# Kernel tuning notes

Hardware: AMD Instinct MI355X
Metric: run time of the kernel (lower is better)

The kernel has to match this reference:

```python
import jax, jax.numpy as jnp
import numpy as np

B, S, HID, NH = 2, 2048, 1024, 16
HD = HID // NH
BASE = 10000.0


def _rope_tables(seq_len, head_dim):
    i = jnp.arange(0, head_dim, 2, dtype=jnp.float32)
    theta = BASE ** (-i / head_dim)
    pos = jnp.arange(seq_len, dtype=jnp.float32)
    m_theta = jnp.outer(pos, theta)  # [S, HD/2]
    cos = jnp.repeat(jnp.cos(m_theta), 2, axis=1)  # [S, HD]
    sin = jnp.repeat(jnp.sin(m_theta), 2, axis=1)
    return cos, sin


def _apply_rope(x, cos, sin):
    # x: [B, NH, S, HD]; interleaved rotation: (-x1, x0, -x3, x2, ...)
    x_even = x[..., 0::2]
    x_odd = x[..., 1::2]
    inv_x = jnp.stack((-x_odd, x_even), axis=-1).reshape(x.shape)
    return x * cos[None, None] + inv_x * sin[None, None]


def setup_inputs() -> dict:
    key = jax.random.key(0)
    ks = jax.random.split(key, 7)
    q = jax.random.normal(ks[0], (B, S, HID), dtype=jnp.float32)
    k = jax.random.normal(ks[1], (B, S, HID), dtype=jnp.float32)
    v = jax.random.normal(ks[2], (B, S, HID), dtype=jnp.float32)
    scale = 1.0 / np.sqrt(HID)
    Wq = jax.random.normal(ks[3], (HID, HID), dtype=jnp.float32) * scale
    Wk = jax.random.normal(ks[4], (HID, HID), dtype=jnp.float32) * scale
    Wv = jax.random.normal(ks[5], (HID, HID), dtype=jnp.float32) * scale
    Wo = jax.random.normal(ks[6], (HID, HID), dtype=jnp.float32) * scale
    mask = jnp.triu(jnp.ones((S, S), dtype=bool), k=1)[None, None]  # causal, True = masked
    return {"q": q, "k": k, "v": v, "mask": mask,
            "Wq": Wq, "Wk": Wk, "Wv": Wv, "Wo": Wo}


def reference(q, k, v, mask, Wq, Wk, Wv, Wo):
    cos, sin = _rope_tables(S, HD)
    # Linear (torch stores weight as [out, in]; y = x @ W.T)
    qh = (q @ Wq.T).reshape(B, S, NH, HD).transpose(0, 2, 1, 3)
    kh = (k @ Wk.T).reshape(B, S, NH, HD).transpose(0, 2, 1, 3)
    vh = (v @ Wv.T).reshape(B, S, NH, HD).transpose(0, 2, 1, 3)
    qh = _apply_rope(qh, cos, sin)
    kh = _apply_rope(kh, cos, sin)
    scores = jnp.einsum("bhqd,bhkd->bhqk", qh, kh) / np.sqrt(HD)
    neg_min = jnp.finfo(jnp.float32).min
    scores = jnp.where(mask, neg_min, scores)
    attn = jax.nn.softmax(scores, axis=-1)
    out = jnp.einsum("bhqk,bhkd->bhqd", attn, vh)  # [B,NH,S,HD]
    out = out.transpose(0, 2, 1, 3).reshape(B, S, HID)
    return out @ Wo.T
```

## Files before the change

kernel.cpp:

```cpp
#include <hip/hip_runtime.h>

#define S_LEN 2048
#define HIDN  1024
#define NHEAD 16
#define HDIM  64
#define MROWS 4096
#define KDIM  1024
#define NDIM  1024

typedef __attribute__((ext_vector_type(8))) short bf16x8;
typedef __attribute__((ext_vector_type(4))) short bf16x4;
typedef __attribute__((ext_vector_type(4))) float f32x4;

static __device__ __forceinline__ ushort f2bf(float f) {
    unsigned int u = __float_as_uint(f);
    u = (u + 0x7fffu + ((u >> 16) & 1u)) >> 16;
    return (ushort)u;
}
static __device__ __forceinline__ float bf2f(ushort u) {
    return __uint_as_float(((unsigned int)u) << 16);
}

static __device__ __forceinline__ void gload16(const ushort* g, ushort* l) {
    __builtin_amdgcn_global_load_lds(
        (const __attribute__((address_space(1))) unsigned int*)g,
        (__attribute__((address_space(3))) unsigned int*)l, 16, 0, 0);
}

__global__ __launch_bounds__(256) void prep_kernel(
    const float* __restrict__ q, const float* __restrict__ k,
    const float* __restrict__ v, const float* __restrict__ Wq,
    const float* __restrict__ Wk, const float* __restrict__ Wv,
    const float* __restrict__ Wo,
    ushort* __restrict__ qb, ushort* __restrict__ kb, ushort* __restrict__ vb,
    ushort* __restrict__ Wqb, ushort* __restrict__ Wkb, ushort* __restrict__ Wvb,
    ushort* __restrict__ Wob,
    float* __restrict__ rc, float* __restrict__ rs)
{
    const long Q4 = (long)MROWS * KDIM / 4;
    const long W4 = (long)NDIM * KDIM / 4;
    if (blockIdx.x < 16384) {
        long i = (long)blockIdx.x * 256 + threadIdx.x;
        const float* src; ushort* dst; long off;
        if (i < Q4)          { src = q; dst = qb; off = i; }
        else if (i < 2 * Q4) { src = k; dst = kb; off = i - Q4; }
        else if (i < 3 * Q4) { src = v; dst = vb; off = i - 2 * Q4; }
        else {
            long t = i - 3 * Q4;
            int wsel = (int)(t >> 18);
            off = t & (W4 - 1);
            src = (wsel == 0) ? Wq : (wsel == 1) ? Wk : (wsel == 2) ? Wv : Wo;
            dst = (wsel == 0) ? Wqb : (wsel == 1) ? Wkb : (wsel == 2) ? Wvb : Wob;
        }
        float4 vv = ((const float4*)src)[off];
        ushort4 o;
        o.x = f2bf(vv.x); o.y = f2bf(vv.y); o.z = f2bf(vv.z); o.w = f2bf(vv.w);
        ((ushort4*)dst)[off] = o;
    } else {
        int idx = (blockIdx.x - 16384) * 256 + threadIdx.x;
        int s  = idx >> 5;
        int jp = idx & 31;
        float theta = expf(-(float)(2 * jp) * (9.210340371976184f / 64.0f));
        float ang = (float)s * theta;
        float sv, cv;
        sincosf(ang, &sv, &cv);
        rc[idx] = cv;
        rs[idx] = sv;
    }
}

static __device__ __forceinline__ void gemm_mainloop128(
    const ushort* __restrict__ A, const ushort* __restrict__ W,
    ushort* As, ushort* Bs, f32x4 (&acc)[4][4],
    int m0, int n0, int tid)
{
    const int lane = tid & 63, wid = tid >> 6;
    const int wm = wid & 1, wn = wid >> 1;
    const int quad = lane >> 4, l15 = lane & 15;

    for (int k0 = 0; k0 < KDIM; k0 += 64) {
        __syncthreads();
#pragma unroll
        for (int rr = 0; rr < 4; ++rr) {
            int sidx = tid + rr * 256;
            int row = sidx >> 3;
            int g = (sidx & 7) ^ (row & 7);
            gload16(A + (size_t)(m0 + row) * KDIM + k0 + g * 8, As + sidx * 8);
            gload16(W + (size_t)(n0 + row) * KDIM + k0 + g * 8, Bs + sidx * 8);
        }
        __syncthreads();

#pragma unroll
        for (int ks = 0; ks < 2; ++ks) {
            bf16x8 af[4], bfr[4];
#pragma unroll
            for (int i = 0; i < 4; ++i) {
                int row = wm * 64 + i * 16 + l15;
                int gg = ((ks << 2) | quad) ^ (row & 7);
                af[i] = *(const bf16x8*)&As[row * 64 + gg * 8];
            }
#pragma unroll
            for (int j = 0; j < 4; ++j) {
                int row = wn * 64 + j * 16 + l15;
                int gg = ((ks << 2) | quad) ^ (row & 7);
                bfr[j] = *(const bf16x8*)&Bs[row * 64 + gg * 8];
            }
#pragma unroll
            for (int i = 0; i < 4; ++i)
#pragma unroll
                for (int j = 0; j < 4; ++j)
                    acc[i][j] = __builtin_amdgcn_mfma_f32_16x16x32_bf16(
                        af[i], bfr[j], acc[i][j], 0, 0, 0);
        }
    }
}

__global__ __launch_bounds__(256, 3) void gemm_qkv(
    const ushort* __restrict__ qb, const ushort* __restrict__ kb,
    const ushort* __restrict__ vb,
    const ushort* __restrict__ Wqb, const ushort* __restrict__ Wkb,
    const ushort* __restrict__ Wvb,
    ushort* __restrict__ Qh, ushort* __restrict__ Kh, ushort* __restrict__ Vt,
    const float* __restrict__ rc, const float* __restrict__ rs)
{
    __shared__ __align__(16) ushort As[128 * 64];
    __shared__ __align__(16) ushort Bs[128 * 64];

    const int tid = threadIdx.x;
    const int lane = tid & 63, wid = tid >> 6;
    const int wm = wid & 1, wn = wid >> 1;
    const int quad = lane >> 4, l15 = lane & 15;
    const int z = blockIdx.z;

    const ushort* A; const ushort* W; int m0, n0;
    if (z == 2) {
        m0 = (int)blockIdx.y * 128;
        n0 = (int)blockIdx.x * 128;
        A = Wvb; W = vb;
    } else {
        m0 = blockIdx.x * 128; n0 = blockIdx.y * 128;
        A = (z == 0) ? qb : kb;
        W = (z == 0) ? Wqb : Wkb;
    }

    f32x4 acc[4][4];
#pragma unroll
    for (int i = 0; i < 4; ++i)
#pragma unroll
        for (int j = 0; j < 4; ++j) acc[i][j] = 0.0f;

    gemm_mainloop128(A, W, As, Bs, acc, m0, n0, tid);

    if (z != 2) {
        ushort* out = (z == 0) ? Qh : Kh;
        const float scale = (z == 0) ? 0.18033688011112042f : 1.0f;
#pragma unroll
        for (int i = 0; i < 4; ++i)
#pragma unroll
            for (int j = 0; j < 4; ++j)
#pragma unroll
                for (int r = 0; r < 4; ++r) {
                    int m = m0 + wm * 64 + i * 16 + quad * 4 + r;
                    int n = n0 + wn * 64 + j * 16 + l15;
                    float v = acc[i][j][r];
                    int b = m >> 11, s = m & (S_LEN - 1);
                    int h = n >> 6, d = n & 63;
                    int pidx = s * 32 + (d >> 1);
                    float cv = rc[pidx], sv = rs[pidx];
                    float partner = __shfl_xor(v, 1);
                    v = (d & 1) ? (v * cv + partner * sv)
                                : (v * cv - partner * sv);
                    out[((size_t)((b * NHEAD + h) * S_LEN + s)) * HDIM + d] =
                        f2bf(v * scale);
                }
    } else {
#pragma unroll
        for (int i = 0; i < 4; ++i)
#pragma unroll
            for (int j = 0; j < 4; ++j)
#pragma unroll
                for (int r = 0; r < 4; ++r) {
                    int m = m0 + wm * 64 + i * 16 + quad * 4 + r;
                    int n = n0 + wn * 64 + j * 16 + l15;
                    int h = m >> 6, d = m & 63;
                    int b = n >> 11, s = n & (S_LEN - 1);
                    Vt[((size_t)((b * NHEAD + h) * HDIM + d)) * S_LEN + s] =
                        f2bf(acc[i][j][r]);
                }
    }
}

__global__ __launch_bounds__(256) void gemm_out(
    const ushort* __restrict__ O0, const ushort* __restrict__ O1,
    const float* __restrict__ L0, const float* __restrict__ L1,
    const ushort* __restrict__ W, float* __restrict__ out)
{
    __shared__ __align__(16) ushort As[64 * 64];
    __shared__ __align__(16) ushort Bs[128 * 64];

    const int tid = threadIdx.x;
    const int lane = tid & 63, wid = tid >> 6;
    const int wm = wid & 1, wn = wid >> 1;
    const int quad = lane >> 4, l15 = lane & 15;
    const int m0 = blockIdx.x * 64, n0 = blockIdx.y * 128;

    f32x4 acc[2][4];
#pragma unroll
    for (int i = 0; i < 2; ++i)
#pragma unroll
        for (int j = 0; j < 4; ++j) acc[i][j] = 0.0f;

    for (int k0 = 0; k0 < KDIM; k0 += 64) {
        const int h = k0 >> 6;
        bf16x8 a0[2], a1[2];
        float li[2];
#pragma unroll
        for (int rr = 0; rr < 2; ++rr) {
            int sidx = tid + rr * 256;
            int row = sidx >> 3;
            int g = (sidx & 7) ^ (row & 7);
            int m = m0 + row, bb = m >> 11, s = m & (S_LEN - 1);
            size_t rowO = (size_t)(bb * NHEAD + h) * S_LEN + s;
            a0[rr] = *(const bf16x8*)(O0 + rowO * HDIM + g * 8);
            a1[rr] = *(const bf16x8*)(O1 + rowO * HDIM + g * 8);
            li[rr] = __builtin_amdgcn_rcpf(L0[rowO] + L1[rowO]);
        }
        __syncthreads();
#pragma unroll
        for (int rr = 0; rr < 2; ++rr) {
            int sidx = tid + rr * 256;
            bf16x8 packed;
#pragma unroll
            for (int e = 0; e < 8; ++e) {
                float f = (bf2f((ushort)a0[rr][e]) + bf2f((ushort)a1[rr][e])) * li[rr];
                packed[e] = (short)(__float_as_uint(f) >> 16);
            }
            *(bf16x8*)&As[sidx * 8] = packed;
        }
#pragma unroll
        for (int rr = 0; rr < 4; ++rr) {
            int sidx = tid + rr * 256;
            int row = sidx >> 3;
            int g = (sidx & 7) ^ (row & 7);
            gload16(W + (size_t)(n0 + row) * KDIM + k0 + g * 8, Bs + sidx * 8);
        }
        __syncthreads();

#pragma unroll
        for (int ks = 0; ks < 2; ++ks) {
            bf16x8 af[2], bfr[4];
#pragma unroll
            for (int i = 0; i < 2; ++i) {
                int row = wm * 32 + i * 16 + l15;
                int gg = ((ks << 2) | quad) ^ (row & 7);
                af[i] = *(const bf16x8*)&As[row * 64 + gg * 8];
            }
#pragma unroll
            for (int j = 0; j < 4; ++j) {
                int row = wn * 64 + j * 16 + l15;
                int gg = ((ks << 2) | quad) ^ (row & 7);
                bfr[j] = *(const bf16x8*)&Bs[row * 64 + gg * 8];
            }
#pragma unroll
            for (int i = 0; i < 2; ++i)
#pragma unroll
                for (int j = 0; j < 4; ++j)
                    acc[i][j] = __builtin_amdgcn_mfma_f32_16x16x32_bf16(
                        af[i], bfr[j], acc[i][j], 0, 0, 0);
        }
    }

#pragma unroll
    for (int i = 0; i < 2; ++i)
#pragma unroll
        for (int j = 0; j < 4; ++j)
#pragma unroll
            for (int r = 0; r < 4; ++r) {
                int m = m0 + wm * 32 + i * 16 + quad * 4 + r;
                int n = n0 + wn * 64 + j * 16 + l15;
                out[(size_t)m * NDIM + n] = acc[i][j][r];
            }
}

__global__ __launch_bounds__(256) void attn_mfma(
    const ushort* __restrict__ Qh, const ushort* __restrict__ Kh,
    const ushort* __restrict__ Vt,
    ushort* __restrict__ O0, ushort* __restrict__ O1,
    float* __restrict__ L0, float* __restrict__ L1)
{
    __shared__ __align__(16) ushort Ks[64 * 64];
    __shared__ __align__(16) ushort Vs[64 * 64];

    const int tid = threadIdx.x;
    const int lane = tid & 63, w = tid >> 6;
    const int quad = lane >> 4, l15 = lane & 15;
    const int id = blockIdx.x;
    const int h = id & 15, b = (id >> 4) & 1, t = id >> 5;

    int seg, y;
    if (t < 32) { seg = (t & 1) ? 0 : 1; y = (t & 1) ? 31 - (t >> 1) : (t >> 1); }
    else { int u = t - 32; seg = (u & 1) ? 0 : 1;
           y = (u & 1) ? 15 - (u >> 1) : 16 + (u >> 1); }

    const int qt = seg ? (31 - y) : y;
    const int lo = seg ? ((33 - y) >> 1) : 0;
    const int hi = seg ? (32 - y) : ((y + 2) >> 1);
    const int q0 = qt * 64;
    const size_t hoff = (size_t)(b * NHEAD + h) * S_LEN * HDIM;

    bf16x8 qf[2];
#pragma unroll
    for (int ks = 0; ks < 2; ++ks)
        qf[ks] = *(const bf16x8*)(Qh + hoff +
            (size_t)(q0 + w * 16 + l15) * HDIM + ks * 32 + quad * 8);

    f32x4 Oa[4];
#pragma unroll
    for (int mt = 0; mt < 4; ++mt) Oa[mt] = 0.0f;
    float lsum = 0.f;
    const int myq = q0 + w * 16 + l15;

    const ushort* kg[2];
    const ushort* vgr[2];
    int vwa[2][2];
#pragma unroll
    for (int rr = 0; rr < 2; ++rr) {
        int sidx = tid + rr * 256;
        int row = sidx >> 3;
        int gsw = (sidx & 7) ^ (row & 7);
        kg[rr] = Kh + hoff + (size_t)(lo * 64 + row) * HDIM + gsw * 8;
        int sp = sidx & 7;
        vgr[rr] = Vt + hoff + (size_t)row * S_LEN + lo * 64 + sp * 8;
        vwa[rr][0] = row * 64 + ((2 * sp)     ^ (row & 15)) * 4;
        vwa[rr][1] = row * 64 + ((2 * sp + 1) ^ (row & 15)) * 4;
    }

    bf16x8 vv[2];
    if (lo < hi) {
#pragma unroll
        for (int rr = 0; rr < 2; ++rr) { vv[rr] = *(const bf16x8*)vgr[rr]; vgr[rr] += 64; }
    }

    for (int kt = lo; kt < hi; ++kt) {
        const int k0 = kt * 64;
        const bool diag = (kt == qt);
        __syncthreads();
#pragma unroll
        for (int rr = 0; rr < 2; ++rr) {
            *(bf16x4*)&Vs[vwa[rr][0]] =
                __builtin_shufflevector(vv[rr], vv[rr], 0, 1, 2, 3);
            *(bf16x4*)&Vs[vwa[rr][1]] =
                __builtin_shufflevector(vv[rr], vv[rr], 4, 5, 6, 7);
            gload16(kg[rr], Ks + (tid + rr * 256) * 8);
            kg[rr] += 64 * HDIM;
        }
        if (kt + 1 < hi) {
#pragma unroll
            for (int rr = 0; rr < 2; ++rr) { vv[rr] = *(const bf16x8*)vgr[rr]; vgr[rr] += 64; }
        }
        __syncthreads();

        f32x4 Sa[4];
#pragma unroll
        for (int jm = 0; jm < 4; ++jm) Sa[jm] = 0.0f;
        __builtin_amdgcn_s_setprio(1);
#pragma unroll
        for (int ks = 0; ks < 2; ++ks) {
            const int p = ((ks << 2) | quad) ^ (l15 & 7);
            bf16x8 kf[4];
#pragma unroll
            for (int jm = 0; jm < 4; ++jm)
                kf[jm] = *(const bf16x8*)&Ks[(jm * 16 + l15) * 64 + p * 8];
#pragma unroll
            for (int jm = 0; jm < 4; ++jm)
                Sa[jm] = __builtin_amdgcn_mfma_f32_16x16x32_bf16(
                    kf[jm], qf[ks], Sa[jm], 0, 0, 0);
        }
        __builtin_amdgcn_s_setprio(0);

        bf16x4 pb[4];
#pragma unroll
        for (int jm = 0; jm < 4; ++jm) {
#pragma unroll
            for (int r = 0; r < 4; ++r) {
                float pv = __builtin_amdgcn_exp2f(Sa[jm][r]);
                if (diag) {
                    int key = k0 + jm * 16 + quad * 4 + r;
                    if (key > myq) pv = 0.f;
                }
                lsum += pv;
                pb[jm][r] = (short)(__float_as_uint(pv) >> 16);
            }
        }

        __builtin_amdgcn_s_setprio(1);
#pragma unroll
        for (int jm = 0; jm < 4; ++jm) {
            const int slot = (((jm * 4 + quad) ^ l15) << 2);
#pragma unroll
            for (int mt = 0; mt < 4; ++mt) {
                bf16x4 vf = *(const bf16x4*)&Vs[(mt * 16 + l15) * 64 + slot];
                Oa[mt] = __builtin_amdgcn_mfma_f32_16x16x16bf16_1k(vf, pb[jm],
                                                                   Oa[mt], 0, 0, 0);
            }
        }
        __builtin_amdgcn_s_setprio(0);
    }

    lsum += __shfl_xor(lsum, 16);
    lsum += __shfl_xor(lsum, 32);

    ushort* Op = seg ? O1 : O0;
    float*  Lp = seg ? L1 : L0;
    const size_t row = (size_t)(b * NHEAD + h) * S_LEN + myq;
#pragma unroll
    for (int mt = 0; mt < 4; ++mt) {
        ushort4 o;
        o.x = f2bf(Oa[mt][0]); o.y = f2bf(Oa[mt][1]);
        o.z = f2bf(Oa[mt][2]); o.w = f2bf(Oa[mt][3]);
        *(ushort4*)&Op[row * HDIM + mt * 16 + quad * 4] = o;
    }
    if (quad == 0) Lp[row] = lsum;
}

extern "C" void kernel_launch(void* const* d_in, const int* in_sizes, int n_in,
                              void* d_out, int out_size, void* d_ws, size_t ws_size,
                              hipStream_t stream) {
    const float* qf  = (const float*)d_in[0];
    const float* kf  = (const float*)d_in[1];
    const float* vf  = (const float*)d_in[2];
    const float* Wqf = (const float*)d_in[4];
    const float* Wkf = (const float*)d_in[5];
    const float* Wvf = (const float*)d_in[6];
    const float* Wof = (const float*)d_in[7];
    float* out = (float*)d_out;

    char* wsp = (char*)d_ws;
    float* rc = (float*)wsp;            wsp += 65536 * 4;
    float* rs = (float*)wsp;            wsp += 65536 * 4;
    ushort* qb  = (ushort*)wsp;         wsp += (size_t)MROWS * KDIM * 2;
    ushort* kb  = (ushort*)wsp;         wsp += (size_t)MROWS * KDIM * 2;
    ushort* vb  = (ushort*)wsp;         wsp += (size_t)MROWS * KDIM * 2;
    ushort* Wqb = (ushort*)wsp;         wsp += (size_t)NDIM * KDIM * 2;
    ushort* Wkb = (ushort*)wsp;         wsp += (size_t)NDIM * KDIM * 2;
    ushort* Wvb = (ushort*)wsp;         wsp += (size_t)NDIM * KDIM * 2;
    ushort* Wob = (ushort*)wsp;         wsp += (size_t)NDIM * KDIM * 2;
    ushort* Qh  = (ushort*)wsp;         wsp += (size_t)MROWS * HIDN * 2;
    ushort* Kh  = (ushort*)wsp;         wsp += (size_t)MROWS * HIDN * 2;
    ushort* Vt  = (ushort*)wsp;

    ushort* O0 = qb;
    ushort* O1 = kb;
    float*  L0 = (float*)vb;
    float*  L1 = (float*)vb + 65536;

    prep_kernel<<<16640, 256, 0, stream>>>(qf, kf, vf, Wqf, Wkf, Wvf, Wof,
                                           qb, kb, vb, Wqb, Wkb, Wvb, Wob, rc, rs);

    gemm_qkv<<<dim3(32, 8, 3), 256, 0, stream>>>(
        qb, kb, vb, Wqb, Wkb, Wvb, Qh, Kh, Vt, rc, rs);

    attn_mfma<<<2048, 256, 0, stream>>>(Qh, Kh, Vt, O0, O1, L0, L1);

    gemm_out<<<dim3(64, 8), 256, 0, stream>>>(O0, O1, L0, L1, Wob, out);
}
```

Measured before the change: 207.5 us.

## Split attention tile across waves by query and key halves with LDS reduction

Each of the four waves now handles 32 queries × 32 keys instead of 16 queries × 64 keys. Each K fragment read from LDS is reused by two query tiles and each V fragment by two P tiles, which halves LDS fragment reads per MFMA. The two key-half partial outputs and row sums are combined at the end through an LDS scratch area that reuses the K/V buffers, at the cost of an extra sync and reduction. Launch bounds now also request 4 blocks per CU.

```diff
diff --git a/kernel.cpp b/kernel.cpp
--- a/kernel.cpp
+++ b/kernel.cpp
@@ -282,17 +282,20 @@
             }
 }
 
-__global__ __launch_bounds__(256) void attn_mfma(
+__global__ __launch_bounds__(256, 4) void attn_mfma(
     const ushort* __restrict__ Qh, const ushort* __restrict__ Kh,
     const ushort* __restrict__ Vt,
     ushort* __restrict__ O0, ushort* __restrict__ O1,
     float* __restrict__ L0, float* __restrict__ L1)
 {
-    __shared__ __align__(16) ushort Ks[64 * 64];
-    __shared__ __align__(16) ushort Vs[64 * 64];
+    __shared__ __align__(16) ushort KV[2][64 * 64];
+    __shared__ float lred[4][2][16];
+    ushort* Ks = KV[0];
+    ushort* Vs = KV[1];
 
     const int tid = threadIdx.x;
     const int lane = tid & 63, w = tid >> 6;
+    const int wq = w & 1, wk = w >> 1;
     const int quad = lane >> 4, l15 = lane & 15;
     const int id = blockIdx.x;
     const int h = id & 15, b = (id >> 4) & 1, t = id >> 5;
@@ -308,17 +311,22 @@
     const int q0 = qt * 64;
     const size_t hoff = (size_t)(b * NHEAD + h) * S_LEN * HDIM;
 
-    bf16x8 qf[2];
-#pragma unroll
-    for (int ks = 0; ks < 2; ++ks)
-        qf[ks] = *(const bf16x8*)(Qh + hoff +
-            (size_t)(q0 + w * 16 + l15) * HDIM + ks * 32 + quad * 8);
-
-    f32x4 Oa[4];
-#pragma unroll
-    for (int mt = 0; mt < 4; ++mt) Oa[mt] = 0.0f;
-    float lsum = 0.f;
-    const int myq = q0 + w * 16 + l15;
+    bf16x8 qf[2][2];
+#pragma unroll
+    for (int qn = 0; qn < 2; ++qn)
+#pragma unroll
+        for (int ks = 0; ks < 2; ++ks)
+            qf[qn][ks] = *(const bf16x8*)(Qh + hoff +
+                (size_t)(q0 + wq * 32 + qn * 16 + l15) * HDIM + ks * 32 + quad * 8);
+
+    const int myq0 = q0 + wq * 32 + l15;
+
+    f32x4 Oa[4][2];
+#pragma unroll
+    for (int mt = 0; mt < 4; ++mt)
+#pragma unroll
+        for (int qn = 0; qn < 2; ++qn) Oa[mt][qn] = 0.0f;
+    float lsum[2] = {0.f, 0.f};
 
     const ushort* kg[2];
     const ushort* vgr[2];
@@ -360,67 +368,104 @@
         }
         __syncthreads();
 
-        f32x4 Sa[4];
-#pragma unroll
-        for (int jm = 0; jm < 4; ++jm) Sa[jm] = 0.0f;
+        f32x4 Sa[2][2];
+#pragma unroll
+        for (int jm = 0; jm < 2; ++jm)
+#pragma unroll
+            for (int qn = 0; qn < 2; ++qn) Sa[jm][qn] = 0.0f;
         __builtin_amdgcn_s_setprio(1);
 #pragma unroll
         for (int ks = 0; ks < 2; ++ks) {
             const int p = ((ks << 2) | quad) ^ (l15 & 7);
-            bf16x8 kf[4];
-#pragma unroll
-            for (int jm = 0; jm < 4; ++jm)
-                kf[jm] = *(const bf16x8*)&Ks[(jm * 16 + l15) * 64 + p * 8];
-#pragma unroll
-            for (int jm = 0; jm < 4; ++jm)
-                Sa[jm] = __builtin_amdgcn_mfma_f32_16x16x32_bf16(
-                    kf[jm], qf[ks], Sa[jm], 0, 0, 0);
+            bf16x8 kf[2];
+#pragma unroll
+            for (int jm = 0; jm < 2; ++jm)
+                kf[jm] = *(const bf16x8*)&Ks[(wk * 32 + jm * 16 + l15) * 64 + p * 8];
+#pragma unroll
+            for (int jm = 0; jm < 2; ++jm)
+#pragma unroll
+                for (int qn = 0; qn < 2; ++qn)
+                    Sa[jm][qn] = __builtin_amdgcn_mfma_f32_16x16x32_bf16(
+                        kf[jm], qf[qn][ks], Sa[jm][qn], 0, 0, 0);
         }
         __builtin_amdgcn_s_setprio(0);
 
-        bf16x4 pb[4];
-#pragma unroll
-        for (int jm = 0; jm < 4; ++jm) {
-#pragma unroll
-            for (int r = 0; r < 4; ++r) {
-                float pv = __builtin_amdgcn_exp2f(Sa[jm][r]);
-                if (diag) {
-                    int key = k0 + jm * 16 + quad * 4 + r;
-                    if (key > myq) pv = 0.f;
+        bf16x4 pb[2][2];
+#pragma unroll
+        for (int jm = 0; jm < 2; ++jm)
+#pragma unroll
+            for (int qn = 0; qn < 2; ++qn) {
+                const int mq = myq0 + qn * 16;
+#pragma unroll
+                for (int r = 0; r < 4; ++r) {
+                    float pv = __builtin_amdgcn_exp2f(Sa[jm][qn][r]);
+                    if (diag) {
+                        int key = k0 + wk * 32 + jm * 16 + quad * 4 + r;
+                        if (key > mq) pv = 0.f;
+                    }
+                    lsum[qn] += pv;
+                    pb[jm][qn][r] = (short)(__float_as_uint(pv) >> 16);
                 }
-                lsum += pv;
-                pb[jm][r] = (short)(__float_as_uint(pv) >> 16);
-            }
-        }
+            }
 
         __builtin_amdgcn_s_setprio(1);
 #pragma unroll
-        for (int jm = 0; jm < 4; ++jm) {
-            const int slot = (((jm * 4 + quad) ^ l15) << 2);
+        for (int jm = 0; jm < 2; ++jm) {
+            const int slot = (((wk * 8 + jm * 4 + quad) ^ l15) << 2);
 #pragma unroll
             for (int mt = 0; mt < 4; ++mt) {
                 bf16x4 vf = *(const bf16x4*)&Vs[(mt * 16 + l15) * 64 + slot];
-                Oa[mt] = __builtin_amdgcn_mfma_f32_16x16x16bf16_1k(vf, pb[jm],
-                                                                   Oa[mt], 0, 0, 0);
+#pragma unroll
+                for (int qn = 0; qn < 2; ++qn)
+                    Oa[mt][qn] = __builtin_amdgcn_mfma_f32_16x16x16bf16_1k(
+                        vf, pb[jm][qn], Oa[mt][qn], 0, 0, 0);
             }
         }
         __builtin_amdgcn_s_setprio(0);
     }
 
-    lsum += __shfl_xor(lsum, 16);
-    lsum += __shfl_xor(lsum, 32);
-
-    ushort* Op = seg ? O1 : O0;
-    float*  Lp = seg ? L1 : L0;
-    const size_t row = (size_t)(b * NHEAD + h) * S_LEN + myq;
-#pragma unroll
-    for (int mt = 0; mt < 4; ++mt) {
-        ushort4 o;
-        o.x = f2bf(Oa[mt][0]); o.y = f2bf(Oa[mt][1]);
-        o.z = f2bf(Oa[mt][2]); o.w = f2bf(Oa[mt][3]);
-        *(ushort4*)&Op[row * HDIM + mt * 16 + quad * 4] = o;
-    }
-    if (quad == 0) Lp[row] = lsum;
+#pragma unroll
+    for (int qn = 0; qn < 2; ++qn) {
+        lsum[qn] += __shfl_xor(lsum[qn], 16);
+        lsum[qn] += __shfl_xor(lsum[qn], 32);
+    }
+
+    float* scr = (float*)&KV[0][0];
+    __syncthreads();
+    if (wk == 1) {
+#pragma unroll
+        for (int mt = 0; mt < 4; ++mt)
+#pragma unroll
+            for (int qn = 0; qn < 2; ++qn) {
+                int q32 = qn * 16 + l15;
+                int g = (mt * 4 + quad) ^ l15;
+                *(f32x4*)&scr[wq * 2048 + q32 * 64 + g * 4] = Oa[mt][qn];
+            }
+    }
+    if (quad == 0) { lred[w][0][l15] = lsum[0]; lred[w][1][l15] = lsum[1]; }
+    __syncthreads();
+
+    if (wk == 0) {
+        ushort* Op = seg ? O1 : O0;
+        float*  Lp = seg ? L1 : L0;
+#pragma unroll
+        for (int qn = 0; qn < 2; ++qn) {
+            const size_t row = (size_t)(b * NHEAD + h) * S_LEN + myq0 + qn * 16;
+#pragma unroll
+            for (int mt = 0; mt < 4; ++mt) {
+                int q32 = qn * 16 + l15;
+                int g = (mt * 4 + quad) ^ l15;
+                f32x4 oth = *(const f32x4*)&scr[wq * 2048 + q32 * 64 + g * 4];
+                f32x4 tot = Oa[mt][qn] + oth;
+                ushort4 o;
+                o.x = f2bf(tot[0]); o.y = f2bf(tot[1]);
+                o.z = f2bf(tot[2]); o.w = f2bf(tot[3]);
+                *(ushort4*)&Op[row * HDIM + mt * 16 + quad * 4] = o;
+            }
+            if (quad == 0)
+                Lp[row] = lred[wq][qn][l15] + lred[2 + wq][qn][l15];
+        }
+    }
 }
 
 extern "C" void kernel_launch(void* const* d_in, const int* in_sizes, int n_in,
```

Result: no change. 210.0 us (+1.2%).

## Double-buffer K/V shared tiles in attention loop to overlap loads with MFMA

Applied to the files above, without the earlier changes.

The attention kernel's K and V shared-memory tiles are doubled into two buffers. The next tile's V store and async K global-to-LDS load are issued into the alternate buffer while the current buffer feeds the MFMAs, which leaves one barrier per iteration instead of two. The aim is to hide global load latency behind compute and cut synchronisation. In exchange LDS use per block doubles, which may lower occupancy.

```diff
diff --git a/kernel.cpp b/kernel.cpp
--- a/kernel.cpp
+++ b/kernel.cpp
@@ -288,8 +288,8 @@
     ushort* __restrict__ O0, ushort* __restrict__ O1,
     float* __restrict__ L0, float* __restrict__ L1)
 {
-    __shared__ __align__(16) ushort Ks[64 * 64];
-    __shared__ __align__(16) ushort Vs[64 * 64];
+    __shared__ __align__(16) ushort Ks[2][64 * 64];
+    __shared__ __align__(16) ushort Vs[2][64 * 64];
 
     const int tid = threadIdx.x;
     const int lane = tid & 63, w = tid >> 6;
@@ -339,26 +339,47 @@
     if (lo < hi) {
 #pragma unroll
         for (int rr = 0; rr < 2; ++rr) { vv[rr] = *(const bf16x8*)vgr[rr]; vgr[rr] += 64; }
+#pragma unroll
+        for (int rr = 0; rr < 2; ++rr) {
+            *(bf16x4*)&Vs[0][vwa[rr][0]] =
+                __builtin_shufflevector(vv[rr], vv[rr], 0, 1, 2, 3);
+            *(bf16x4*)&Vs[0][vwa[rr][1]] =
+                __builtin_shufflevector(vv[rr], vv[rr], 4, 5, 6, 7);
+            gload16(kg[rr], &Ks[0][(tid + rr * 256) * 8]);
+            kg[rr] += 64 * HDIM;
+        }
+        if (lo + 1 < hi) {
+#pragma unroll
+            for (int rr = 0; rr < 2; ++rr) { vv[rr] = *(const bf16x8*)vgr[rr]; vgr[rr] += 64; }
+        }
     }
 
     for (int kt = lo; kt < hi; ++kt) {
         const int k0 = kt * 64;
         const bool diag = (kt == qt);
+        const int p = (kt - lo) & 1;
+        const ushort* Ksp = Ks[p];
+        const ushort* Vsp = Vs[p];
+
         __syncthreads();
-#pragma unroll
-        for (int rr = 0; rr < 2; ++rr) {
-            *(bf16x4*)&Vs[vwa[rr][0]] =
-                __builtin_shufflevector(vv[rr], vv[rr], 0, 1, 2, 3);
-            *(bf16x4*)&Vs[vwa[rr][1]] =
-                __builtin_shufflevector(vv[rr], vv[rr], 4, 5, 6, 7);
-            gload16(kg[rr], Ks + (tid + rr * 256) * 8);
-            kg[rr] += 64 * HDIM;
-        }
+
         if (kt + 1 < hi) {
-#pragma unroll
-            for (int rr = 0; rr < 2; ++rr) { vv[rr] = *(const bf16x8*)vgr[rr]; vgr[rr] += 64; }
-        }
-        __syncthreads();
+            ushort* Ksn = Ks[p ^ 1];
+            ushort* Vsn = Vs[p ^ 1];
+#pragma unroll
+            for (int rr = 0; rr < 2; ++rr) {
+                *(bf16x4*)&Vsn[vwa[rr][0]] =
+                    __builtin_shufflevector(vv[rr], vv[rr], 0, 1, 2, 3);
+                *(bf16x4*)&Vsn[vwa[rr][1]] =
+                    __builtin_shufflevector(vv[rr], vv[rr], 4, 5, 6, 7);
+                gload16(kg[rr], &Ksn[(tid + rr * 256) * 8]);
+                kg[rr] += 64 * HDIM;
+            }
+            if (kt + 2 < hi) {
+#pragma unroll
+                for (int rr = 0; rr < 2; ++rr) { vv[rr] = *(const bf16x8*)vgr[rr]; vgr[rr] += 64; }
+            }
+        }
 
         f32x4 Sa[4];
 #pragma unroll
@@ -366,11 +387,11 @@
         __builtin_amdgcn_s_setprio(1);
 #pragma unroll
         for (int ks = 0; ks < 2; ++ks) {
-            const int p = ((ks << 2) | quad) ^ (l15 & 7);
+            const int pp = ((ks << 2) | quad) ^ (l15 & 7);
             bf16x8 kf[4];
 #pragma unroll
             for (int jm = 0; jm < 4; ++jm)
-                kf[jm] = *(const bf16x8*)&Ks[(jm * 16 + l15) * 64 + p * 8];
+                kf[jm] = *(const bf16x8*)&Ksp[(jm * 16 + l15) * 64 + pp * 8];
 #pragma unroll
             for (int jm = 0; jm < 4; ++jm)
                 Sa[jm] = __builtin_amdgcn_mfma_f32_16x16x32_bf16(
@@ -399,7 +420,7 @@
             const int slot = (((jm * 4 + quad) ^ l15) << 2);
 #pragma unroll
             for (int mt = 0; mt < 4; ++mt) {
-                bf16x4 vf = *(const bf16x4*)&Vs[(mt * 16 + l15) * 64 + slot];
+                bf16x4 vf = *(const bf16x4*)&Vsp[(mt * 16 + l15) * 64 + slot];
                 Oa[mt] = __builtin_amdgcn_mfma_f32_16x16x16bf16_1k(vf, pb[jm],
                                                                    Oa[mt], 0, 0, 0);
             }
```

Measured after the change: 217.1 us. +4.6%, slower.
